# Optimization experiments

Hardware: AMD Instinct MI355X
Metric: run time of the kernel (lower is better)

The kernel has to match this reference:

```python
import jax, jax.numpy as jnp
import numpy as np

D_MODEL = 1024
N_HEADS = 16
WINDOW = 64
GLOBAL_RATIO = 0.1
HEAD_DIM = D_MODEL // N_HEADS
NEG_INF = -1e9  # matches torch float32 branch of _get_neg_inf
B, L = 1, 2048


def setup_inputs() -> dict:
    key = jax.random.key(0)
    ks = jax.random.split(key, 6)
    x = jax.random.normal(ks[0], (B, L, D_MODEL), jnp.float32)
    s = 1.0 / np.sqrt(D_MODEL)  # nn.Linear default init bound

    def lin(k):
        k1, k2 = jax.random.split(k)
        W = jax.random.uniform(k1, (D_MODEL, D_MODEL), jnp.float32, -s, s)
        b = jax.random.uniform(k2, (D_MODEL,), jnp.float32, -s, s)
        return W, b

    Wq, bq = lin(ks[1])
    Wk, bk = lin(ks[2])
    Wv, bv = lin(ks[3])
    Wo, bo = lin(ks[4])
    n_global = max(1, int(L * GLOBAL_RATIO))  # 204
    global_indices = jnp.sort(jax.random.randint(ks[5], (n_global,), 0, L))
    return dict(x=x, Wq=Wq, bq=bq, Wk=Wk, bk=bk, Wv=Wv, bv=bv, Wo=Wo, bo=bo,
                global_indices=global_indices)


def reference(x, Wq, bq, Wk, bk, Wv, bv, Wo, bo, global_indices):
    Bb, Ll, Dm = x.shape
    H, Dh = N_HEADS, HEAD_DIM
    scale = 1.0 / jnp.sqrt(jnp.float32(Dh))
    # projections (torch Linear: y = x @ W.T + b)
    Q = (x @ Wq.T + bq).reshape(Bb, Ll, H, Dh)
    K = (x @ Wk.T + bk).reshape(Bb, Ll, H, Dh)
    V = (x @ Wv.T + bv).reshape(Bb, Ll, H, Dh)

    # --- local sliding-window attention (vectorized version of the per-i loop) ---
    half = WINDOW // 2
    W = WINDOW + 1  # positions i-half .. i+half inclusive
    pos = jnp.arange(Ll)[:, None] + jnp.arange(-half, half + 1)[None, :]  # [L,W]
    valid = (pos >= 0) & (pos < Ll)          # edge truncation == masking to -inf
    posc = jnp.clip(pos, 0, Ll - 1)
    Kw = K[:, posc]                           # [B,L,W,H,Dh]
    Vw = V[:, posc]
    s_loc = jnp.einsum('blhd,blwhd->bhlw', Q, Kw) * scale
    s_loc = jnp.where(valid[None, None], s_loc, NEG_INF)
    a_loc = jax.nn.softmax(s_loc, axis=-1)
    local = jnp.einsum('bhlw,blwhd->blhd', a_loc, Vw)

    # --- global random-token attention ---
    Kg = K[:, global_indices]                 # [B,G,H,Dh]
    Vg = V[:, global_indices]
    s_g = jnp.einsum('blhd,bghd->bhlg', Q, Kg) * scale
    a_g = jax.nn.softmax(s_g, axis=-1)
    glob = jnp.einsum('bhlg,bghd->blhd', a_g, Vg)

    out = 0.7 * local + 0.3 * glob
    return out.reshape(Bb, Ll, Dm) @ Wo.T + bo
```

## Files before the change

### kernel.cpp

```cpp
#include <hip/hip_runtime.h>
#include <hip/hip_bf16.h>
#include <stdint.h>

#define L_SEQ 2048
#define D_MODEL 1024
#define NH 16
#define DH 64
#define NEG_INF -1e9f
#define BM 128
#define BN 128
#define BK 32

typedef short bf16x8 __attribute__((ext_vector_type(8)));
typedef float f32x4 __attribute__((ext_vector_type(4)));
typedef unsigned short ushort_t;
typedef const __attribute__((address_space(1))) void* gas_t;
typedef __attribute__((address_space(3))) void* las_t;

#define MFMA16(a, b, c) __builtin_amdgcn_mfma_f32_16x16x32_bf16((a), (b), (c), 0, 0, 0)

__device__ __forceinline__ ushort_t f2b(float f) {
  union { float f; unsigned u; } v; v.f = f;
  unsigned r = v.u + 0x7fffu + ((v.u >> 16) & 1u);
  return (ushort_t)(r >> 16);
}

__global__ __launch_bounds__(256) void cvt_kernel(
    const float* __restrict__ x, const float* __restrict__ wq,
    const float* __restrict__ wk, const float* __restrict__ wv,
    const float* __restrict__ wo, ushort_t* __restrict__ out) {
  long e = ((long)blockIdx.x * 256 + threadIdx.x) * 4;
  const float* src; long off;
  if (e < 2097152L)      { src = x;  off = e; }
  else if (e < 3145728L) { src = wq; off = e - 2097152L; }
  else if (e < 4194304L) { src = wk; off = e - 3145728L; }
  else if (e < 5242880L) { src = wv; off = e - 4194304L; }
  else                   { src = wo; off = e - 5242880L; }
  float4 v = *(const float4*)(src + off);
  ushort4 o;
  o.x = f2b(v.x); o.y = f2b(v.y); o.z = f2b(v.z); o.w = f2b(v.w);
  *(ushort4*)(out + e) = o;
}

__global__ __launch_bounds__(512, 4) void gemm_bt(
    const ushort_t* __restrict__ A, const ushort_t* __restrict__ Wbase,
    const float* __restrict__ b0, const float* __restrict__ b1,
    const float* __restrict__ b2, void* __restrict__ outbase, int mode) {
  const int z = blockIdx.z;
  const ushort_t* W = Wbase + (long)z * (D_MODEL * D_MODEL);
  const float* bias = (z == 0) ? b0 : ((z == 1) ? b1 : b2);
  const float scale = (mode == 0 && z == 0) ? 0.125f : 1.0f;

  __shared__ ushort_t As[4 * BM * BK];
  __shared__ ushort_t Bs[4 * BN * BK];
  const int tid = threadIdx.x;
  const int lane = tid & 63;
  const int wid = tid >> 6;
  const int wm = wid >> 2, wn = wid & 3;
  const int m0 = blockIdx.x * BM, n0 = blockIdx.y * BN;
  const int K = D_MODEL;
  const int l15 = lane & 15, lg8 = (lane >> 4) * 8;

  const int soff = tid * 16;
  const int srow = soff >> 6;
  const int scol = (soff & 63) >> 1;

  const ushort_t* Aptr = A + (long)(m0 + srow) * K + scol;
  const ushort_t* Wptr = W + (long)(n0 + srow) * K + scol;

  auto stage = [&](int buf, int step) {
    __builtin_amdgcn_global_load_lds(
        (gas_t)(const void*)(Aptr + step * BK),
        (las_t)(void*)((char*)As + buf * 8192 + soff), 16, 0, 0);
    __builtin_amdgcn_global_load_lds(
        (gas_t)(const void*)(Wptr + step * BK),
        (las_t)(void*)((char*)Bs + buf * 8192 + soff), 16, 0, 0);
  };

  f32x4 acc[4][2] = {};

  auto compute = [&](int buf) {
    const ushort_t* Ab = As + buf * (BM * BK);
    const ushort_t* Bb = Bs + buf * (BN * BK);
    bf16x8 af[4], bf[2];
#pragma unroll
    for (int t = 0; t < 4; ++t)
      af[t] = *(const bf16x8*)(Ab + (wm * 64 + t * 16 + l15) * BK + lg8);
#pragma unroll
    for (int t = 0; t < 2; ++t)
      bf[t] = *(const bf16x8*)(Bb + (wn * 32 + t * 16 + l15) * BK + lg8);
#pragma unroll
    for (int mt = 0; mt < 4; ++mt)
#pragma unroll
      for (int nt = 0; nt < 2; ++nt)
        acc[mt][nt] = MFMA16(af[mt], bf[nt], acc[mt][nt]);
  };

  const int NSTEP = K / BK;
  stage(0, 0);
  stage(1, 1);
  for (int s = 0; s < NSTEP - 2; ++s) {
    stage((s + 2) & 3, s + 2);
    asm volatile("s_waitcnt vmcnt(4)" ::: "memory");
    __builtin_amdgcn_s_barrier();
    __builtin_amdgcn_sched_barrier(0);
    compute(s & 3);
  }
  asm volatile("s_waitcnt vmcnt(2)" ::: "memory");
  __builtin_amdgcn_s_barrier();
  __builtin_amdgcn_sched_barrier(0);
  compute((NSTEP - 2) & 3);
  asm volatile("s_waitcnt vmcnt(0)" ::: "memory");
  __builtin_amdgcn_s_barrier();
  __builtin_amdgcn_sched_barrier(0);
  compute((NSTEP - 1) & 3);

  const int lg4 = (lane >> 4) * 4;
  if (mode == 0) {
    ushort_t* o = (ushort_t*)outbase + (long)z * ((long)NH * L_SEQ * DH);
#pragma unroll
    for (int mt = 0; mt < 4; ++mt)
#pragma unroll
      for (int nt = 0; nt < 2; ++nt)
#pragma unroll
        for (int r = 0; r < 4; ++r) {
          int row = m0 + wm * 64 + mt * 16 + lg4 + r;
          int col = n0 + wn * 32 + nt * 16 + l15;
          float v = (acc[mt][nt][r] + bias[col]) * scale;
          o[((long)(col >> 6) * L_SEQ + row) * DH + (col & 63)] = f2b(v);
        }
  } else {
    float* o = (float*)outbase;
#pragma unroll
    for (int mt = 0; mt < 4; ++mt)
#pragma unroll
      for (int nt = 0; nt < 2; ++nt)
#pragma unroll
        for (int r = 0; r < 4; ++r) {
          int row = m0 + wm * 64 + mt * 16 + lg4 + r;
          int col = n0 + wn * 32 + nt * 16 + l15;
          o[(long)row * D_MODEL + col] = acc[mt][nt][r] + bias[col];
        }
  }
}

__global__ __launch_bounds__(256) void attn_kernel(
    const ushort_t* __restrict__ QKV, const int* __restrict__ gidx, int NG,
    ushort_t* __restrict__ attn_out) {
  __shared__ ushort_t buf0[128 * 72];
  __shared__ ushort_t buf1[128 * 72];
  __shared__ ushort_t buf2[96 * 72];

  const int tid = threadIdx.x;
  const int lane = tid & 63;
  const int w = tid >> 6;
  const int h = blockIdx.y;
  const int q0 = blockIdx.x * 64;

  const long hoff = (long)h * L_SEQ * DH;
  const ushort_t* Qh = QKV + hoff;
  const ushort_t* Kh = QKV + (long)NH * L_SEQ * DH + hoff;
  const ushort_t* Vh = QKV + 2L * NH * L_SEQ * DH + hoff;

  const int rr = tid >> 3;
  const int c8 = (tid & 7) * 8;

#pragma unroll
  for (int it = 0; it < 4; ++it) {
    int r = rr + it * 32;
    int sr = q0 - 32 + r;
    sr = sr < 0 ? 0 : (sr > L_SEQ - 1 ? L_SEQ - 1 : sr);
    int4 v = *(const int4*)(Kh + (long)sr * DH + c8);
    *(int4*)(buf0 + r * 72 + c8) = v;
  }
#pragma unroll
  for (int it = 0; it < 4; ++it) {
    int r = rr + it * 32;
    int idx = r < NG ? r : NG - 1;
    int4 v = *(const int4*)(Kh + (long)gidx[idx] * DH + c8);
    *(int4*)(buf1 + r * 72 + c8) = v;
  }
#pragma unroll
  for (int it = 0; it < 3; ++it) {
    int r = rr + it * 32;
    int i = 128 + r;
    int idx = i < NG ? i : NG - 1;
    int4 v = *(const int4*)(Kh + (long)gidx[idx] * DH + c8);
    *(int4*)(buf2 + r * 72 + c8) = v;
  }
  __syncthreads();

  const int l15 = lane & 15, lg = lane >> 4;
  const int ql = q0 + w * 16 + l15;
  bf16x8 qf0 = *(const bf16x8*)(Qh + (long)ql * DH + lg * 8);
  bf16x8 qf1 = *(const bf16x8*)(Qh + (long)ql * DH + 32 + lg * 8);

  f32x4 sl[8], sg[14];
#pragma unroll
  for (int kt = 0; kt < 8; ++kt) {
    f32x4 c = {};
    bf16x8 k0 = *(const bf16x8*)(buf0 + (kt * 16 + l15) * 72 + lg * 8);
    bf16x8 k1 = *(const bf16x8*)(buf0 + (kt * 16 + l15) * 72 + 32 + lg * 8);
    c = MFMA16(k0, qf0, c);
    c = MFMA16(k1, qf1, c);
    sl[kt] = c;
  }
#pragma unroll
  for (int kt = 0; kt < 8; ++kt) {
    f32x4 c = {};
    bf16x8 k0 = *(const bf16x8*)(buf1 + (kt * 16 + l15) * 72 + lg * 8);
    bf16x8 k1 = *(const bf16x8*)(buf1 + (kt * 16 + l15) * 72 + 32 + lg * 8);
    c = MFMA16(k0, qf0, c);
    c = MFMA16(k1, qf1, c);
    sg[kt] = c;
  }
#pragma unroll
  for (int kt = 0; kt < 6; ++kt) {
    f32x4 c = {};
    bf16x8 k0 = *(const bf16x8*)(buf2 + (kt * 16 + l15) * 72 + lg * 8);
    bf16x8 k1 = *(const bf16x8*)(buf2 + (kt * 16 + l15) * 72 + 32 + lg * 8);
    c = MFMA16(k0, qf0, c);
    c = MFMA16(k1, qf1, c);
    sg[8 + kt] = c;
  }
  __syncthreads();

  int4 vst[11];
#pragma unroll
  for (int it = 0; it < 4; ++it) {
    int r = rr + it * 32;
    int sr = q0 - 32 + r;
    sr = sr < 0 ? 0 : (sr > L_SEQ - 1 ? L_SEQ - 1 : sr);
    vst[it] = *(const int4*)(Vh + (long)sr * DH + c8);
  }
#pragma unroll
  for (int it = 0; it < 4; ++it) {
    int r = rr + it * 32;
    int idx = r < NG ? r : NG - 1;
    vst[4 + it] = *(const int4*)(Vh + (long)gidx[idx] * DH + c8);
  }
#pragma unroll
  for (int it = 0; it < 3; ++it) {
    int i = 128 + rr + it * 32;
    int idx = i < NG ? i : NG - 1;
    vst[8 + it] = *(const int4*)(Vh + (long)gidx[idx] * DH + c8);
  }

  float mx = NEG_INF;
#pragma unroll
  for (int kt = 0; kt < 8; ++kt)
#pragma unroll
    for (int r4 = 0; r4 < 4; ++r4) {
      int key = q0 - 32 + kt * 16 + lg * 4 + r4;
      int d = key - ql;
      bool valid = (key >= 0) && (key < L_SEQ) && (d <= 32) && (d >= -32);
      float v = valid ? sl[kt][r4] : NEG_INF;
      sl[kt][r4] = v;
      mx = fmaxf(mx, v);
    }
  mx = fmaxf(mx, __shfl_xor(mx, 16, 64));
  mx = fmaxf(mx, __shfl_xor(mx, 32, 64));
  float den = 0.f;
#pragma unroll
  for (int kt = 0; kt < 8; ++kt)
#pragma unroll
    for (int r4 = 0; r4 < 4; ++r4) {
      float e = __expf(sl[kt][r4] - mx);
      sl[kt][r4] = e;
      den += e;
    }
  den += __shfl_xor(den, 16, 64);
  den += __shfl_xor(den, 32, 64);
  const float psl = 0.7f / den;

  float mg = NEG_INF;
#pragma unroll
  for (int t = 0; t < 14; ++t)
#pragma unroll
    for (int r4 = 0; r4 < 4; ++r4) {
      int i = t * 16 + lg * 4 + r4;
      float v = (i < NG) ? sg[t][r4] : NEG_INF;
      sg[t][r4] = v;
      mg = fmaxf(mg, v);
    }
  mg = fmaxf(mg, __shfl_xor(mg, 16, 64));
  mg = fmaxf(mg, __shfl_xor(mg, 32, 64));
  float deng = 0.f;
#pragma unroll
  for (int t = 0; t < 14; ++t)
#pragma unroll
    for (int r4 = 0; r4 < 4; ++r4) {
      float e = __expf(sg[t][r4] - mg);
      sg[t][r4] = e;
      deng += e;
    }
  deng += __shfl_xor(deng, 16, 64);
  deng += __shfl_xor(deng, 32, 64);
  const float psg = 0.3f / deng;

  bf16x8 pl[4], pg[7];
#pragma unroll
  for (int s = 0; s < 4; ++s)
#pragma unroll
    for (int j = 0; j < 4; ++j) {
      pl[s][j]     = (short)f2b(sl[2 * s][j] * psl);
      pl[s][j + 4] = (short)f2b(sl[2 * s + 1][j] * psl);
    }
#pragma unroll
  for (int s = 0; s < 7; ++s)
#pragma unroll
    for (int j = 0; j < 4; ++j) {
      pg[s][j]     = (short)f2b(sg[2 * s][j] * psg);
      pg[s][j + 4] = (short)f2b(sg[2 * s + 1][j] * psg);
    }

#pragma unroll
  for (int it = 0; it < 4; ++it)
    *(int4*)(buf0 + (rr + it * 32) * 72 + c8) = vst[it];
#pragma unroll
  for (int it = 0; it < 4; ++it)
    *(int4*)(buf1 + (rr + it * 32) * 72 + c8) = vst[4 + it];
#pragma unroll
  for (int it = 0; it < 3; ++it)
    *(int4*)(buf2 + (rr + it * 32) * 72 + c8) = vst[8 + it];
  __syncthreads();

  f32x4 o4[4];
#pragma unroll
  for (int dt = 0; dt < 4; ++dt) {
    f32x4 c = {};
    const int dc = dt * 16 + l15;
#pragma unroll
    for (int s = 0; s < 4; ++s) {
      bf16x8 vf;
#pragma unroll
      for (int j = 0; j < 8; ++j) {
        int key = s * 32 + lg * 4 + (j & 3) + 16 * (j >> 2);
        vf[j] = (short)buf0[key * 72 + dc];
      }
      c = MFMA16(pl[s], vf, c);
    }
#pragma unroll
    for (int s = 0; s < 4; ++s) {
      bf16x8 vf;
#pragma unroll
      for (int j = 0; j < 8; ++j) {
        int key = s * 32 + lg * 4 + (j & 3) + 16 * (j >> 2);
        vf[j] = (short)buf1[key * 72 + dc];
      }
      c = MFMA16(pg[s], vf, c);
    }
#pragma unroll
    for (int s = 0; s < 3; ++s) {
      bf16x8 vf;
#pragma unroll
      for (int j = 0; j < 8; ++j) {
        int key = s * 32 + lg * 4 + (j & 3) + 16 * (j >> 2);
        vf[j] = (short)buf2[key * 72 + dc];
      }
      c = MFMA16(pg[4 + s], vf, c);
    }
    o4[dt] = c;
  }

#pragma unroll
  for (int dt = 0; dt < 4; ++dt)
#pragma unroll
    for (int r4 = 0; r4 < 4; ++r4) {
      int row = q0 + w * 16 + lg * 4 + r4;
      int dc = dt * 16 + l15;
      attn_out[(long)row * D_MODEL + h * DH + dc] = f2b(o4[dt][r4]);
    }
}

extern "C" void kernel_launch(void* const* d_in, const int* in_sizes, int n_in,
                              void* d_out, int out_size, void* d_ws, size_t ws_size,
                              hipStream_t stream) {
  const float* x  = (const float*)d_in[0];
  const float* Wq = (const float*)d_in[1];
  const float* bq = (const float*)d_in[2];
  const float* Wk = (const float*)d_in[3];
  const float* bk = (const float*)d_in[4];
  const float* Wv = (const float*)d_in[5];
  const float* bv = (const float*)d_in[6];
  const float* Wo = (const float*)d_in[7];
  const float* bo = (const float*)d_in[8];
  const int* gidx = (const int*)d_in[9];
  const int NG = in_sizes[9];

  ushort_t* ws = (ushort_t*)d_ws;
  ushort_t* xb   = ws;
  ushort_t* wb   = ws + 2097152L;
  ushort_t* qkv  = ws + 6291456L;
  ushort_t* attn = ws + 12582912L;

  cvt_kernel<<<6144, 256, 0, stream>>>(x, Wq, Wk, Wv, Wo, ws);
  gemm_bt<<<dim3(16, 8, 3), 512, 0, stream>>>(xb, wb, bq, bk, bv, qkv, 0);
  attn_kernel<<<dim3(32, 16), 256, 0, stream>>>(qkv, gidx, NG, attn);
  gemm_bt<<<dim3(16, 8, 1), 512, 0, stream>>>(attn, wb + 3145728L, bo, bo, bo,
                                              d_out, 1);
}
```

Before: 65.33 us.

## Transpose V into shared memory and retile the output projection GEMM

```diff
diff --git a/kernel.cpp b/kernel.cpp
--- a/kernel.cpp
+++ b/kernel.cpp
@@ -7,10 +7,8 @@
 #define NH 16
 #define DH 64
 #define NEG_INF -1e9f
-#define BM 128
-#define BN 128
-#define BK 32
-
+
+typedef short bf16x4 __attribute__((ext_vector_type(4)));
 typedef short bf16x8 __attribute__((ext_vector_type(8)));
 typedef float f32x4 __attribute__((ext_vector_type(4)));
 typedef unsigned short ushort_t;
@@ -42,22 +40,22 @@
   *(ushort4*)(out + e) = o;
 }
 
-__global__ __launch_bounds__(512, 4) void gemm_bt(
+__global__ __launch_bounds__(512, 4) void gemm_qkv(
     const ushort_t* __restrict__ A, const ushort_t* __restrict__ Wbase,
     const float* __restrict__ b0, const float* __restrict__ b1,
-    const float* __restrict__ b2, void* __restrict__ outbase, int mode) {
+    const float* __restrict__ b2, ushort_t* __restrict__ outbase) {
   const int z = blockIdx.z;
   const ushort_t* W = Wbase + (long)z * (D_MODEL * D_MODEL);
   const float* bias = (z == 0) ? b0 : ((z == 1) ? b1 : b2);
-  const float scale = (mode == 0 && z == 0) ? 0.125f : 1.0f;
-
-  __shared__ ushort_t As[4 * BM * BK];
-  __shared__ ushort_t Bs[4 * BN * BK];
+  const float scale = (z == 0) ? 0.125f : 1.0f;
+
+  __shared__ ushort_t As[4 * 128 * 32];
+  __shared__ ushort_t Bs[4 * 128 * 32];
   const int tid = threadIdx.x;
   const int lane = tid & 63;
   const int wid = tid >> 6;
   const int wm = wid >> 2, wn = wid & 3;
-  const int m0 = blockIdx.x * BM, n0 = blockIdx.y * BN;
+  const int m0 = blockIdx.x * 128, n0 = blockIdx.y * 128;
   const int K = D_MODEL;
   const int l15 = lane & 15, lg8 = (lane >> 4) * 8;
 
@@ -70,25 +68,25 @@
 
   auto stage = [&](int buf, int step) {
     __builtin_amdgcn_global_load_lds(
-        (gas_t)(const void*)(Aptr + step * BK),
+        (gas_t)(const void*)(Aptr + step * 32),
         (las_t)(void*)((char*)As + buf * 8192 + soff), 16, 0, 0);
     __builtin_amdgcn_global_load_lds(
-        (gas_t)(const void*)(Wptr + step * BK),
+        (gas_t)(const void*)(Wptr + step * 32),
         (las_t)(void*)((char*)Bs + buf * 8192 + soff), 16, 0, 0);
   };
 
   f32x4 acc[4][2] = {};
 
   auto compute = [&](int buf) {
-    const ushort_t* Ab = As + buf * (BM * BK);
-    const ushort_t* Bb = Bs + buf * (BN * BK);
+    const ushort_t* Ab = As + buf * (128 * 32);
+    const ushort_t* Bb = Bs + buf * (128 * 32);
     bf16x8 af[4], bf[2];
 #pragma unroll
     for (int t = 0; t < 4; ++t)
-      af[t] = *(const bf16x8*)(Ab + (wm * 64 + t * 16 + l15) * BK + lg8);
+      af[t] = *(const bf16x8*)(Ab + (wm * 64 + t * 16 + l15) * 32 + lg8);
 #pragma unroll
     for (int t = 0; t < 2; ++t)
-      bf[t] = *(const bf16x8*)(Bb + (wn * 32 + t * 16 + l15) * BK + lg8);
+      bf[t] = *(const bf16x8*)(Bb + (wn * 32 + t * 16 + l15) * 32 + lg8);
 #pragma unroll
     for (int mt = 0; mt < 4; ++mt)
 #pragma unroll
@@ -96,7 +94,7 @@
         acc[mt][nt] = MFMA16(af[mt], bf[nt], acc[mt][nt]);
   };
 
-  const int NSTEP = K / BK;
+  const int NSTEP = K / 32;
   stage(0, 0);
   stage(1, 1);
   for (int s = 0; s < NSTEP - 2; ++s) {
@@ -116,40 +114,109 @@
   compute((NSTEP - 1) & 3);
 
   const int lg4 = (lane >> 4) * 4;
-  if (mode == 0) {
-    ushort_t* o = (ushort_t*)outbase + (long)z * ((long)NH * L_SEQ * DH);
+  ushort_t* o = outbase + (long)z * ((long)NH * L_SEQ * DH);
+#pragma unroll
+  for (int mt = 0; mt < 4; ++mt)
+#pragma unroll
+    for (int nt = 0; nt < 2; ++nt)
+#pragma unroll
+      for (int r = 0; r < 4; ++r) {
+        int row = m0 + wm * 64 + mt * 16 + lg4 + r;
+        int col = n0 + wn * 32 + nt * 16 + l15;
+        float v = (acc[mt][nt][r] + bias[col]) * scale;
+        o[((long)(col >> 6) * L_SEQ + row) * DH + (col & 63)] = f2b(v);
+      }
+}
+
+__global__ __launch_bounds__(256, 3) void gemm_out(
+    const ushort_t* __restrict__ A, const ushort_t* __restrict__ W,
+    const float* __restrict__ bias, float* __restrict__ o) {
+  __shared__ ushort_t As[4 * 128 * 32];
+  __shared__ ushort_t Bs[4 * 64 * 32];
+  const int tid = threadIdx.x;
+  const int lane = tid & 63;
+  const int wid = tid >> 6;
+  const int wm = wid >> 1, wn = wid & 1;
+  const int m0 = blockIdx.x * 128, n0 = blockIdx.y * 64;
+  const int K = D_MODEL;
+  const int l15 = lane & 15, lg8 = (lane >> 4) * 8;
+
+  const int soff = tid * 16;
+  const int srow = soff >> 6;
+  const int scol = (soff & 63) >> 1;
+
+  const ushort_t* Aptr0 = A + (long)(m0 + srow) * K + scol;
+  const ushort_t* Aptr1 = A + (long)(m0 + 64 + srow) * K + scol;
+  const ushort_t* Wptr  = W + (long)(n0 + srow) * K + scol;
+
+  auto stage = [&](int buf, int step) {
+    __builtin_amdgcn_global_load_lds(
+        (gas_t)(const void*)(Aptr0 + step * 32),
+        (las_t)(void*)((char*)As + buf * 8192 + soff), 16, 0, 0);
+    __builtin_amdgcn_global_load_lds(
+        (gas_t)(const void*)(Aptr1 + step * 32),
+        (las_t)(void*)((char*)As + buf * 8192 + 4096 + soff), 16, 0, 0);
+    __builtin_amdgcn_global_load_lds(
+        (gas_t)(const void*)(Wptr + step * 32),
+        (las_t)(void*)((char*)Bs + buf * 4096 + soff), 16, 0, 0);
+  };
+
+  f32x4 acc[4][2] = {};
+
+  auto compute = [&](int buf) {
+    const ushort_t* Ab = As + buf * (128 * 32);
+    const ushort_t* Bb = Bs + buf * (64 * 32);
+    bf16x8 af[4], bf[2];
+#pragma unroll
+    for (int t = 0; t < 4; ++t)
+      af[t] = *(const bf16x8*)(Ab + (wm * 64 + t * 16 + l15) * 32 + lg8);
+#pragma unroll
+    for (int t = 0; t < 2; ++t)
+      bf[t] = *(const bf16x8*)(Bb + (wn * 32 + t * 16 + l15) * 32 + lg8);
 #pragma unroll
     for (int mt = 0; mt < 4; ++mt)
 #pragma unroll
       for (int nt = 0; nt < 2; ++nt)
-#pragma unroll
-        for (int r = 0; r < 4; ++r) {
-          int row = m0 + wm * 64 + mt * 16 + lg4 + r;
-          int col = n0 + wn * 32 + nt * 16 + l15;
-          float v = (acc[mt][nt][r] + bias[col]) * scale;
-          o[((long)(col >> 6) * L_SEQ + row) * DH + (col & 63)] = f2b(v);
-        }
-  } else {
-    float* o = (float*)outbase;
-#pragma unroll
-    for (int mt = 0; mt < 4; ++mt)
-#pragma unroll
-      for (int nt = 0; nt < 2; ++nt)
-#pragma unroll
-        for (int r = 0; r < 4; ++r) {
-          int row = m0 + wm * 64 + mt * 16 + lg4 + r;
-          int col = n0 + wn * 32 + nt * 16 + l15;
-          o[(long)row * D_MODEL + col] = acc[mt][nt][r] + bias[col];
-        }
-  }
-}
-
+        acc[mt][nt] = MFMA16(af[mt], bf[nt], acc[mt][nt]);
+  };
+
+  const int NSTEP = K / 32;
+  stage(0, 0);
+  stage(1, 1);
+  for (int s = 0; s < NSTEP - 2; ++s) {
+    stage((s + 2) & 3, s + 2);
+    asm volatile("s_waitcnt vmcnt(6)" ::: "memory");
+    __builtin_amdgcn_s_barrier();
+    __builtin_amdgcn_sched_barrier(0);
+    compute(s & 3);
+  }
+  asm volatile("s_waitcnt vmcnt(3)" ::: "memory");
+  __builtin_amdgcn_s_barrier();
+  __builtin_amdgcn_sched_barrier(0);
+  compute((NSTEP - 2) & 3);
+  asm volatile("s_waitcnt vmcnt(0)" ::: "memory");
+  __builtin_amdgcn_s_barrier();
+  __builtin_amdgcn_sched_barrier(0);
+  compute((NSTEP - 1) & 3);
+
+  const int lg4 = (lane >> 4) * 4;
+#pragma unroll
+  for (int mt = 0; mt < 4; ++mt)
+#pragma unroll
+    for (int nt = 0; nt < 2; ++nt)
+#pragma unroll
+      for (int r = 0; r < 4; ++r) {
+        int row = m0 + wm * 64 + mt * 16 + lg4 + r;
+        int col = n0 + wn * 32 + nt * 16 + l15;
+        o[(long)row * D_MODEL + col] = acc[mt][nt][r] + bias[col];
+      }
+}
+
+#define STK 356
 __global__ __launch_bounds__(256) void attn_kernel(
     const ushort_t* __restrict__ QKV, const int* __restrict__ gidx, int NG,
     ushort_t* __restrict__ attn_out) {
-  __shared__ ushort_t buf0[128 * 72];
-  __shared__ ushort_t buf1[128 * 72];
-  __shared__ ushort_t buf2[96 * 72];
+  __shared__ ushort_t smem[352 * 72];
 
   const int tid = threadIdx.x;
   const int lane = tid & 63;
@@ -165,20 +232,24 @@
   const int rr = tid >> 3;
   const int c8 = (tid & 7) * 8;
 
+  ushort_t* kb0 = smem;
+  ushort_t* kb1 = smem + 128 * 72;
+  ushort_t* kb2 = smem + 256 * 72;
+
 #pragma unroll
   for (int it = 0; it < 4; ++it) {
     int r = rr + it * 32;
     int sr = q0 - 32 + r;
     sr = sr < 0 ? 0 : (sr > L_SEQ - 1 ? L_SEQ - 1 : sr);
     int4 v = *(const int4*)(Kh + (long)sr * DH + c8);
-    *(int4*)(buf0 + r * 72 + c8) = v;
+    *(int4*)(kb0 + r * 72 + c8) = v;
   }
 #pragma unroll
   for (int it = 0; it < 4; ++it) {
     int r = rr + it * 32;
     int idx = r < NG ? r : NG - 1;
     int4 v = *(const int4*)(Kh + (long)gidx[idx] * DH + c8);
-    *(int4*)(buf1 + r * 72 + c8) = v;
+    *(int4*)(kb1 + r * 72 + c8) = v;
   }
 #pragma unroll
   for (int it = 0; it < 3; ++it) {
@@ -186,7 +257,7 @@
     int i = 128 + r;
     int idx = i < NG ? i : NG - 1;
     int4 v = *(const int4*)(Kh + (long)gidx[idx] * DH + c8);
-    *(int4*)(buf2 + r * 72 + c8) = v;
+    *(int4*)(kb2 + r * 72 + c8) = v;
   }
   __syncthreads();
 
@@ -199,8 +270,8 @@
 #pragma unroll
   for (int kt = 0; kt < 8; ++kt) {
     f32x4 c = {};
-    bf16x8 k0 = *(const bf16x8*)(buf0 + (kt * 16 + l15) * 72 + lg * 8);
-    bf16x8 k1 = *(const bf16x8*)(buf0 + (kt * 16 + l15) * 72 + 32 + lg * 8);
+    bf16x8 k0 = *(const bf16x8*)(kb0 + (kt * 16 + l15) * 72 + lg * 8);
+    bf16x8 k1 = *(const bf16x8*)(kb0 + (kt * 16 + l15) * 72 + 32 + lg * 8);
     c = MFMA16(k0, qf0, c);
     c = MFMA16(k1, qf1, c);
     sl[kt] = c;
@@ -208,8 +279,8 @@
 #pragma unroll
   for (int kt = 0; kt < 8; ++kt) {
     f32x4 c = {};
-    bf16x8 k0 = *(const bf16x8*)(buf1 + (kt * 16 + l15) * 72 + lg * 8);
-    bf16x8 k1 = *(const bf16x8*)(buf1 + (kt * 16 + l15) * 72 + 32 + lg * 8);
+    bf16x8 k0 = *(const bf16x8*)(kb1 + (kt * 16 + l15) * 72 + lg * 8);
+    bf16x8 k1 = *(const bf16x8*)(kb1 + (kt * 16 + l15) * 72 + 32 + lg * 8);
     c = MFMA16(k0, qf0, c);
     c = MFMA16(k1, qf1, c);
     sg[kt] = c;
@@ -217,8 +288,8 @@
 #pragma unroll
   for (int kt = 0; kt < 6; ++kt) {
     f32x4 c = {};
-    bf16x8 k0 = *(const bf16x8*)(buf2 + (kt * 16 + l15) * 72 + lg * 8);
-    bf16x8 k1 = *(const bf16x8*)(buf2 + (kt * 16 + l15) * 72 + 32 + lg * 8);
+    bf16x8 k0 = *(const bf16x8*)(kb2 + (kt * 16 + l15) * 72 + lg * 8);
+    bf16x8 k1 = *(const bf16x8*)(kb2 + (kt * 16 + l15) * 72 + 32 + lg * 8);
     c = MFMA16(k0, qf0, c);
     c = MFMA16(k1, qf1, c);
     sg[8 + kt] = c;
@@ -315,50 +386,39 @@
     }
 
 #pragma unroll
-  for (int it = 0; it < 4; ++it)
-    *(int4*)(buf0 + (rr + it * 32) * 72 + c8) = vst[it];
-#pragma unroll
-  for (int it = 0; it < 4; ++it)
-    *(int4*)(buf1 + (rr + it * 32) * 72 + c8) = vst[4 + it];
-#pragma unroll
-  for (int it = 0; it < 3; ++it)
-    *(int4*)(buf2 + (rr + it * 32) * 72 + c8) = vst[8 + it];
+  for (int it = 0; it < 4; ++it) {
+    int r = rr + it * 32;
+    ushort_t tmp[8]; *(int4*)tmp = vst[it];
+#pragma unroll
+    for (int j = 0; j < 8; ++j) smem[(c8 + j) * STK + r] = tmp[j];
+  }
+#pragma unroll
+  for (int it = 0; it < 4; ++it) {
+    int r = 128 + rr + it * 32;
+    ushort_t tmp[8]; *(int4*)tmp = vst[4 + it];
+#pragma unroll
+    for (int j = 0; j < 8; ++j) smem[(c8 + j) * STK + r] = tmp[j];
+  }
+#pragma unroll
+  for (int it = 0; it < 3; ++it) {
+    int r = 256 + rr + it * 32;
+    ushort_t tmp[8]; *(int4*)tmp = vst[8 + it];
+#pragma unroll
+    for (int j = 0; j < 8; ++j) smem[(c8 + j) * STK + r] = tmp[j];
+  }
   __syncthreads();
 
   f32x4 o4[4];
 #pragma unroll
   for (int dt = 0; dt < 4; ++dt) {
     f32x4 c = {};
-    const int dc = dt * 16 + l15;
-#pragma unroll
-    for (int s = 0; s < 4; ++s) {
-      bf16x8 vf;
-#pragma unroll
-      for (int j = 0; j < 8; ++j) {
-        int key = s * 32 + lg * 4 + (j & 3) + 16 * (j >> 2);
-        vf[j] = (short)buf0[key * 72 + dc];
-      }
-      c = MFMA16(pl[s], vf, c);
-    }
-#pragma unroll
-    for (int s = 0; s < 4; ++s) {
-      bf16x8 vf;
-#pragma unroll
-      for (int j = 0; j < 8; ++j) {
-        int key = s * 32 + lg * 4 + (j & 3) + 16 * (j >> 2);
-        vf[j] = (short)buf1[key * 72 + dc];
-      }
-      c = MFMA16(pg[s], vf, c);
-    }
-#pragma unroll
-    for (int s = 0; s < 3; ++s) {
-      bf16x8 vf;
-#pragma unroll
-      for (int j = 0; j < 8; ++j) {
-        int key = s * 32 + lg * 4 + (j & 3) + 16 * (j >> 2);
-        vf[j] = (short)buf2[key * 72 + dc];
-      }
-      c = MFMA16(pg[4 + s], vf, c);
+    const ushort_t* vrow = smem + (dt * 16 + l15) * STK + lg * 4;
+#pragma unroll
+    for (int s = 0; s < 11; ++s) {
+      bf16x4 lo = *(const bf16x4*)(vrow + s * 32);
+      bf16x4 hi = *(const bf16x4*)(vrow + s * 32 + 16);
+      bf16x8 vf = __builtin_shufflevector(lo, hi, 0, 1, 2, 3, 4, 5, 6, 7);
+      c = MFMA16(s < 4 ? pl[s] : pg[s - 4], vf, c);
     }
     o4[dt] = c;
   }
@@ -395,8 +455,8 @@
   ushort_t* attn = ws + 12582912L;
 
   cvt_kernel<<<6144, 256, 0, stream>>>(x, Wq, Wk, Wv, Wo, ws);
-  gemm_bt<<<dim3(16, 8, 3), 512, 0, stream>>>(xb, wb, bq, bk, bv, qkv, 0);
+  gemm_qkv<<<dim3(16, 8, 3), 512, 0, stream>>>(xb, wb, bq, bk, bv, qkv);
   attn_kernel<<<dim3(32, 16), 256, 0, stream>>>(qkv, gidx, NG, attn);
-  gemm_bt<<<dim3(16, 8, 1), 512, 0, stream>>>(attn, wb + 3145728L, bo, bo, bo,
-                                              d_out, 1);
-}
+  gemm_out<<<dim3(16, 16), 256, 0, stream>>>(attn, wb + 3145728L, bo,
+                                             (float*)d_out);
+}
```

New measurement: 65.57 us. No clear change (+0.4%).
